# Optimization experiments

Measured on AMD Instinct MI355X. Metric: run time of the kernel, lower is better.

## Reference

```python
import jax, jax.numpy as jnp
import numpy as np

K_CAND = 64
K_FINAL = 16
ALPHA = 0.5
CURV_RATIO = 0.5
EPS = 1e-8


def index_points(points, idx):
    # points: [B, N, C], idx: [B, ...] -> [B, ..., C]
    B, N, C = points.shape
    flat = idx.reshape(B, -1)
    g = jnp.take_along_axis(points, flat[..., None], axis=1)
    return g.reshape(idx.shape + (C,))


def fps(points, num_fps):
    # Furthest point sampling (matches pointnet2: starts from index 0).
    B, N, _ = points.shape
    barange = jnp.arange(B)

    def body(carry, _):
        mindist, last_idx = carry
        last_pt = points[barange, last_idx]                       # [B, 3]
        d = jnp.sum((points - last_pt[:, None, :]) ** 2, axis=-1)  # [B, N]
        mindist = jnp.minimum(mindist, d)
        next_idx = jnp.argmax(mindist, axis=1).astype(jnp.int32)
        return (mindist, next_idx), last_idx

    init = (jnp.full((B, N), 1e10, points.dtype), jnp.zeros((B,), jnp.int32))
    _, idxs = jax.lax.scan(body, init, None, length=num_fps)
    return idxs.T  # [B, num_fps]


def znorm(x):
    # per-cloud normalization over points dim, unbiased std like torch
    return (x - x.mean(axis=1, keepdims=True)) / (x.std(axis=1, ddof=1, keepdims=True) + EPS)


def reference(xyz, features, w1, b1, w2, b2, num_samples):
    B, N, _ = xyz.shape
    # --- candidate kNN via pairwise squared distances (same ordering as cdist) ---
    sq = jnp.sum(xyz * xyz, axis=-1)                               # [B, N]
    d2 = sq[:, :, None] + sq[:, None, :] - 2.0 * jnp.einsum('bnc,bmc->bnm', xyz, xyz)
    _, cand = jax.lax.top_k(-d2, K_CAND + 1)                       # smallest dists first
    cand = cand[:, :, 1:]                                          # drop self -> [B, N, 64]

    # --- learned neighbor scoring MLP on relative geometry/features ---
    nxyz = index_points(xyz, cand)                                 # [B, N, 64, 3]
    nfeat = index_points(features, cand)                           # [B, N, 64, C]
    rel_xyz = nxyz - xyz[:, :, None, :]
    rel_feat = nfeat - features[:, :, None, :]
    mlp_in = jnp.concatenate([rel_xyz, rel_feat], axis=-1)         # [B, N, 64, 3+C]
    h = jax.nn.gelu(mlp_in @ w1 + b1, approximate=False)
    scores = (h @ w2 + b2)[..., 0]                                 # [B, N, 64]
    _, top_in_cand = jax.lax.top_k(scores, K_FINAL)
    final_idx = jnp.take_along_axis(cand, top_in_cand, axis=2)     # [B, N, 16]

    # --- robust importance: curvature (3x3 SVD of cov) + feature variation ---
    n2xyz = index_points(xyz, final_idx)                           # [B, N, 16, 3]
    n2feat = index_points(features, final_idx)
    dxyz = n2xyz - xyz[:, :, None, :]
    cov = jnp.einsum('bnki,bnkj->bnij', dxyz, dxyz) / K_FINAL      # [B, N, 3, 3]
    s = jnp.linalg.svd(cov, compute_uv=False)                      # descending, [B, N, 3]
    l2, l1, l0 = s[..., 0] ** 2, s[..., 1] ** 2, s[..., 2] ** 2
    curvature = l0 / (l0 + l1 + l2 + EPS)
    dfeat = n2feat - features[:, :, None, :]
    feat_var = jnp.linalg.norm(dfeat, axis=-1).mean(axis=-1)       # [B, N]
    importance = znorm(curvature) + ALPHA * znorm(feat_var)

    # --- select curvature points, mask them, FPS for the rest ---
    num_curv = int(num_samples * CURV_RATIO)
    num_fps = num_samples - num_curv
    _, curv_idx = jax.lax.top_k(importance, num_curv)              # [B, num_curv]
    far_val = jnp.max(xyz) + 1.0
    barange = jnp.arange(B)[:, None]
    masked_xyz = xyz.at[barange, curv_idx].set(far_val)
    fps_idx = fps(masked_xyz, num_fps).astype(curv_idx.dtype)      # [B, num_fps]
    merged = jnp.concatenate([curv_idx, fps_idx], axis=1)          # [B, num_samples]
    sampled_xyz = index_points(xyz, merged)                        # [B, num_samples, 3]
    return sampled_xyz, merged


def setup_inputs() -> dict:
    key = jax.random.key(0)
    k1, k2, k3, k4 = jax.random.split(key, 4)
    B, N, C = 2, 8192, 64
    xyz = jax.random.normal(k1, (B, N, 3), jnp.float32)
    features = jax.random.normal(k2, (B, N, C), jnp.float32)
    fan_in1 = 3 + C
    w1 = jax.random.normal(k3, (fan_in1, 128), jnp.float32) / np.sqrt(fan_in1)
    b1 = jnp.zeros((128,), jnp.float32)
    w2 = jax.random.normal(k4, (128, 1), jnp.float32) / np.sqrt(128)
    b2 = jnp.zeros((1,), jnp.float32)
    return {"xyz": xyz, "features": features, "w1": w1, "b1": b1,
            "w2": w2, "b2": b2, "num_samples": 2048}
```

## Files before the change

### kernel.cpp

```cpp
#include <hip/hip_runtime.h>
#include <hip/hip_bf16.h>
#include <math.h>

#define N 8192
#define BATCH 2
#define NROWS (BATCH*N)

typedef float v2f __attribute__((ext_vector_type(2)));

static __device__ __forceinline__ float fsubr(float a, float b){ return __fadd_rn(a, -b); }
static __device__ __forceinline__ unsigned okey(float f){
  unsigned u = __float_as_uint(f);
  return (u & 0x80000000u) ? ~u : (u | 0x80000000u);
}

__global__ void aux_kernel(const float* __restrict__ xyz, float* __restrict__ xs, float* __restrict__ ys,
                           float* __restrict__ zs, float* __restrict__ sq, float4* __restrict__ mxyz){
  int i = blockIdx.x*256 + threadIdx.x;
  if (i < NROWS){
    float x = xyz[i*3+0], y = xyz[i*3+1], z = xyz[i*3+2];
    xs[i]=x; ys[i]=y; zs[i]=z;
    sq[i] = __fadd_rn(__fadd_rn(__fmul_rn(x,x),__fmul_rn(y,y)),__fmul_rn(z,z));
    mxyz[i] = make_float4(x, y, z, 0.0f);
  }
}

__global__ void farval_kernel(const float* __restrict__ xyz, float* __restrict__ farval){
  __shared__ float lm[4];
  float m = -1e30f;
  for (int i = threadIdx.x; i < NROWS*3; i += 256) m = fmaxf(m, xyz[i]);
  for (int off = 32; off; off >>= 1) m = fmaxf(m, __shfl_down(m, off));
  if ((threadIdx.x & 63) == 0) lm[threadIdx.x >> 6] = m;
  __syncthreads();
  if (threadIdx.x == 0){
    float r = fmaxf(fmaxf(lm[0],lm[1]), fmaxf(lm[2],lm[3]));
    farval[0] = __fadd_rn(r, 1.0f);
  }
}

__global__ __launch_bounds__(128) void q_kernel(const float* __restrict__ xyz, const float* __restrict__ feat,
                                                const float* __restrict__ w1, float* __restrict__ Q){
  __shared__ float sx[16][3];
  __shared__ float sf[16][64];
  const int t = threadIdx.x;
  const int row0 = blockIdx.x * 16;
  for (int j = t; j < 1024; j += 128) sf[j>>6][j&63] = feat[(size_t)row0*64 + j];
  if (t < 48) sx[t/3][t%3] = xyz[(size_t)row0*3 + t];
  __syncthreads();
  float acc[16];
  #pragma unroll
  for (int r = 0; r < 16; ++r) acc[r] = 0.0f;
  for (int c = 0; c < 3; ++c){
    float wv = w1[c*128 + t];
    #pragma unroll
    for (int r = 0; r < 16; ++r) acc[r] = fmaf(sx[r][c], wv, acc[r]);
  }
  for (int c = 0; c < 64; ++c){
    float wv = w1[(3+c)*128 + t];
    #pragma unroll
    for (int r = 0; r < 16; ++r) acc[r] = fmaf(sf[r][c], wv, acc[r]);
  }
  #pragma unroll
  for (int r = 0; r < 16; ++r) Q[(size_t)(row0+r)*128 + t] = acc[r];
}

__global__ __launch_bounds__(512) void knn_kernel(const float* __restrict__ xs, const float* __restrict__ ys,
                                                  const float* __restrict__ zs, const float* __restrict__ sq,
                                                  int* __restrict__ cand){
#pragma clang fp contract(off)
  __shared__ unsigned fk[N];
  __shared__ unsigned hist[2048];
  __shared__ unsigned long long win[1024];
  __shared__ int scal[8];
  const int t = threadIdx.x;
  const int base_row = blockIdx.x * 32;
  const int b = base_row >> 13;
  const int n0 = base_row & (N-1);
  const int pbase = b * N;
  v2f px[8], py[8], pz[8], ps[8];
  #pragma unroll
  for (int k = 0; k < 8; ++k){
    int i0 = t + (2*k)*512, i1 = t + (2*k+1)*512;
    px[k].x = xs[pbase+i0]; px[k].y = xs[pbase+i1];
    py[k].x = ys[pbase+i0]; py[k].y = ys[pbase+i1];
    pz[k].x = zs[pbase+i0]; pz[k].y = zs[pbase+i1];
    ps[k].x = sq[pbase+i0]; ps[k].y = sq[pbase+i1];
  }
  for (int r = 0; r < 32; ++r){
    const int n = n0 + r;
    const float qx = xs[pbase+n], qy = ys[pbase+n], qz = zs[pbase+n], qs = sq[pbase+n];
    #pragma unroll
    for (int j = 0; j < 4; ++j) hist[t + j*512] = 0;
    __syncthreads();
    #pragma unroll
    for (int k = 0; k < 8; ++k){
      v2f dot = px[k]*qx + py[k]*qy + pz[k]*qz;
      v2f dd  = (qs + ps[k]) - 2.0f*dot;
      unsigned u0 = okey(dd.x), u1 = okey(dd.y);
      fk[t + (2*k)*512] = u0;
      fk[t + (2*k+1)*512] = u1;
      atomicAdd(&hist[u0 >> 21], 1u);
      atomicAdd(&hist[u1 >> 21], 1u);
    }
    __syncthreads();
    if (t < 64){
      unsigned s = 0;
      for (int k2 = 0; k2 < 32; ++k2) s += hist[t*32 + ((k2 + t) & 31)];
      unsigned p = s;
      for (int off = 1; off < 64; off <<= 1){ unsigned v = (unsigned)__shfl_up((int)p, off); if (t >= off) p += v; }
      int excl = (int)(p - s);
      if (excl < 65 && (int)p >= 65){ scal[0] = t; scal[1] = excl; }
    }
    __syncthreads();
    {
      int g = scal[0];
      if (t < 32){
        unsigned s = hist[g*32 + t];
        unsigned p = s;
        for (int off = 1; off < 32; off <<= 1){ unsigned v = (unsigned)__shfl_up((int)p, off); if (t >= off) p += v; }
        int before = scal[1] + (int)(p - s);
        if (before < 65 && scal[1] + (int)p >= 65) scal[2] = g*32 + t;
      }
    }
    if (t == 0) scal[3] = 0;
    __syncthreads();
    unsigned B1 = (unsigned)scal[2];
    unsigned limit = (B1 >= 2047u) ? 0xFFFFFFFFu : ((B1+1u) << 21);
    #pragma unroll
    for (int j = 0; j < 16; ++j){
      int i = t + j*512;
      unsigned u = fk[i];
      if (u < limit){
        int p = atomicAdd(&scal[3], 1);
        if (p < 1024) win[p] = ((unsigned long long)u << 32) | (unsigned)i;
      }
    }
    __syncthreads();
    int m = scal[3]; if (m > 1024) m = 1024;
    for (int e = t; e < m; e += 512){
      unsigned long long me = win[e];
      int rk = 0;
      for (int j2 = 0; j2 < m; ++j2) rk += (win[j2] < me) ? 1 : 0;
      if (rk >= 1 && rk < 65) cand[(size_t)(pbase + n)*64 + (rk-1)] = (int)(me & 0xFFFFFFFFull);
    }
    __syncthreads();
  }
}

__global__ __launch_bounds__(256) void score_kernel(const float* __restrict__ xyz, const float* __restrict__ feat,
                                                    const float* __restrict__ Q, const float* __restrict__ b1,
                                                    const float* __restrict__ w2, const float* __restrict__ b2,
                                                    const int* __restrict__ cand,
                                                    float* __restrict__ curv, float* __restrict__ fv){
  __shared__ float4 sb14[32], sw24[32];
  __shared__ int ssel[4][16];
  __shared__ float sdx[4][16], sdy[4][16], sdz[4][16], snrm[4][16];
  const int t = threadIdx.x;
  if (t < 32) sb14[t] = ((const float4*)b1)[t];
  else if (t < 64) sw24[t-32] = ((const float4*)w2)[t-32];
  __syncthreads();
  const int w = t >> 6, lane = t & 63;
  const int row = blockIdx.x*4 + w;
  const int b = row >> 13;
  const int pbase = b * N;
  const int n = row & (N-1);
  const int ck = cand[(size_t)row*64 + lane];
  const float4* Qn4 = (const float4*)(Q + (size_t)row * 128);
  const float4* Qc4 = (const float4*)(Q + (size_t)(pbase + ck) * 128);
  const float ks = 0.70710678118654752440f;
  float acc = 0.0f;
  for (int c = 0; c < 32; ++c){
    float4 qc = Qc4[c], qn = Qn4[c], bb = sb14[c], ww = sw24[c];
    float p0 = (qc.x - qn.x) + bb.x;
    float g0 = 0.5f * p0 * (1.0f + erff(p0 * ks));
    acc += g0 * ww.x;
    float p1 = (qc.y - qn.y) + bb.y;
    float g1 = 0.5f * p1 * (1.0f + erff(p1 * ks));
    acc += g1 * ww.y;
    float p2 = (qc.z - qn.z) + bb.z;
    float g2 = 0.5f * p2 * (1.0f + erff(p2 * ks));
    acc += g2 * ww.z;
    float p3 = (qc.w - qn.w) + bb.w;
    float g3 = 0.5f * p3 * (1.0f + erff(p3 * ks));
    acc += g3 * ww.w;
  }
  float score = acc + b2[0];
  unsigned key = okey(score);
  int rk = 0;
  for (int j = 0; j < 64; ++j){
    unsigned kj = (unsigned)__shfl((int)key, j);
    rk += (kj > key || (kj == key && j < lane)) ? 1 : 0;
  }
  float cx = xyz[(size_t)(pbase+ck)*3+0], cy = xyz[(size_t)(pbase+ck)*3+1], cz = xyz[(size_t)(pbase+ck)*3+2];
  float qxv = xyz[(size_t)(pbase+n)*3+0], qyv = xyz[(size_t)(pbase+n)*3+1], qzv = xyz[(size_t)(pbase+n)*3+2];
  if (rk < 16){
    ssel[w][rk] = ck;
    sdx[w][rk] = fsubr(cx, qxv);
    sdy[w][rk] = fsubr(cy, qyv);
    sdz[w][rk] = fsubr(cz, qzv);
  }
  __syncthreads();
  if (lane < 16){
    int si = ssel[w][lane];
    const float4* fc4 = (const float4*)(feat + (size_t)(pbase+si)*64);
    const float4* fn4 = (const float4*)(feat + (size_t)(pbase+n)*64);
    double s = 0.0;
    for (int c = 0; c < 16; ++c){
      float4 a = fc4[c], bq = fn4[c];
      float d0 = fsubr(a.x, bq.x); s += (double)d0 * (double)d0;
      float d1 = fsubr(a.y, bq.y); s += (double)d1 * (double)d1;
      float d2 = fsubr(a.z, bq.z); s += (double)d2 * (double)d2;
      float d3 = fsubr(a.w, bq.w); s += (double)d3 * (double)d3;
    }
    snrm[w][lane] = sqrtf((float)s);
  }
  __syncthreads();
  if (lane == 0){
    double cxx=0, cxy=0, cxz=0, cyy=0, cyz=0, czz=0;
    for (int k2 = 0; k2 < 16; ++k2){
      double dx = (double)sdx[w][k2], dy = (double)sdy[w][k2], dz = (double)sdz[w][k2];
      cxx += dx*dx; cxy += dx*dy; cxz += dx*dz; cyy += dy*dy; cyz += dy*dz; czz += dz*dz;
    }
    float fxx = (float)(cxx/16.0), fxy = (float)(cxy/16.0), fxz = (float)(cxz/16.0);
    float fyy = (float)(cyy/16.0), fyz = (float)(cyz/16.0), fzz = (float)(czz/16.0);
    double a = fxx, bbv = fyy, c = fzz, d = fxy, e = fyz, f = fxz;
    double p1 = d*d + f*f + e*e;
    double e0, e1, e2v;
    if (p1 == 0.0){ e0 = a; e1 = bbv; e2v = c; }
    else {
      double q = (a + bbv + c) / 3.0;
      double aa = a - q, bq = bbv - q, cc = c - q;
      double p2 = aa*aa + bq*bq + cc*cc + 2.0*p1;
      double p = sqrt(p2 / 6.0);
      double inv = 1.0 / p;
      double bxx = aa*inv, byy = bq*inv, bzz = cc*inv, bxy = d*inv, bxz = f*inv, byz = e*inv;
      double detB = bxx*(byy*bzz - byz*byz) - bxy*(bxy*bzz - byz*bxz) + bxz*(bxy*byz - byy*bxz);
      double rr = 0.5 * detB;
      rr = fmin(1.0, fmax(-1.0, rr));
      double phi = acos(rr) / 3.0;
      e0 = q + 2.0*p*cos(phi);
      e2v = q + 2.0*p*cos(phi + 2.0943951023931953);
      e1 = 3.0*q - e0 - e2v;
    }
    double s0 = fabs(e0), s1 = fabs(e1), s2d = fabs(e2v), tt;
    if (s0 < s1){ tt=s0; s0=s1; s1=tt; }
    if (s1 < s2d){ tt=s1; s1=s2d; s2d=tt; }
    if (s0 < s1){ tt=s0; s0=s1; s1=tt; }
    float sv0 = (float)s0, sv1 = (float)s1, sv2 = (float)s2d;
    float l2f = __fmul_rn(sv0,sv0), l1f = __fmul_rn(sv1,sv1), l0f = __fmul_rn(sv2,sv2);
    float den = __fadd_rn(__fadd_rn(__fadd_rn(l0f, l1f), l2f), 1e-8f);
    curv[row] = l0f / den;
    double fs = 0.0;
    for (int k2 = 0; k2 < 16; ++k2) fs += (double)snrm[w][k2];
    fv[row] = (float)(fs / 16.0);
  }
}

static __device__ __forceinline__ double blk_sum(double v, double* lds, int t){
  for (int off = 32; off; off >>= 1) v += __shfl_down(v, off);
  int w = t >> 6, lane = t & 63;
  if (lane == 0) lds[w] = v;
  __syncthreads();
  double r = (t < 16) ? lds[t] : 0.0;
  if (t < 64){ for (int off = 8; off; off >>= 1) r += __shfl_down(r, off); }
  if (t == 0) lds[0] = r;
  __syncthreads();
  double out = lds[0];
  __syncthreads();
  return out;
}

__global__ __launch_bounds__(1024) void stats_kernel(const float* __restrict__ curv, const float* __restrict__ fv,
                                                     float* __restrict__ imp){
  __shared__ double lds[16];
  const int t = threadIdx.x;
  const int base = blockIdx.x * N;
  double sc = 0, sf = 0;
  for (int j = 0; j < 8; ++j){ int i = t + j*1024; sc += (double)curv[base+i]; sf += (double)fv[base+i]; }
  double Sc = blk_sum(sc, lds, t);
  double Sf = blk_sum(sf, lds, t);
  double mc = Sc/8192.0, mf = Sf/8192.0;
  double vc = 0, vf = 0;
  for (int j = 0; j < 8; ++j){ int i = t + j*1024;
    double d1 = (double)curv[base+i] - mc; vc += d1*d1;
    double d2 = (double)fv[base+i]  - mf; vf += d2*d2; }
  double Vc = blk_sum(vc, lds, t);
  double Vf = blk_sum(vf, lds, t);
  float mcf = (float)mc, mff = (float)mf;
  float dc = __fadd_rn((float)sqrt(Vc/8191.0), 1e-8f);
  float df = __fadd_rn((float)sqrt(Vf/8191.0), 1e-8f);
  for (int j = 0; j < 8; ++j){ int i = t + j*1024;
    float zc = fsubr(curv[base+i], mcf) / dc;
    float zf = fsubr(fv[base+i],  mff) / df;
    imp[base+i] = __fadd_rn(zc, __fmul_rn(0.5f, zf));
  }
}

__global__ __launch_bounds__(1024) void topk_kernel(const float* __restrict__ imp, int* __restrict__ merged,
                                                    float4* __restrict__ mxyz, const float* __restrict__ farval){
  __shared__ unsigned dk[N];
  __shared__ unsigned hist[2048];
  __shared__ unsigned long long win[2048];
  __shared__ int scal[8];
  const int t = threadIdx.x;
  const int b = blockIdx.x;
  const int base = b * N;
  #pragma unroll
  for (int j = 0; j < 2; ++j) hist[t + j*1024] = 0;
  if (t == 0) scal[3] = 0;
  __syncthreads();
  for (int j = 0; j < 8; ++j){
    int i = t + j*1024;
    unsigned u = ~okey(imp[base+i]);
    dk[i] = u;
    atomicAdd(&hist[u >> 21], 1u);
  }
  __syncthreads();
  if (t < 64){
    unsigned s = 0;
    for (int k2 = 0; k2 < 32; ++k2) s += hist[t*32 + ((k2 + t) & 31)];
    unsigned p = s;
    for (int off = 1; off < 64; off <<= 1){ unsigned v = (unsigned)__shfl_up((int)p, off); if (t >= off) p += v; }
    int excl = (int)(p - s);
    if (excl < 1024 && (int)p >= 1024){ scal[0] = t; scal[1] = excl; }
  }
  __syncthreads();
  {
    int g = scal[0];
    if (t < 32){
      unsigned s = hist[g*32 + t];
      unsigned p = s;
      for (int off = 1; off < 32; off <<= 1){ unsigned v = (unsigned)__shfl_up((int)p, off); if (t >= off) p += v; }
      int before = scal[1] + (int)(p - s);
      if (before < 1024 && scal[1] + (int)p >= 1024) scal[2] = g*32 + t;
    }
  }
  __syncthreads();
  unsigned B1 = (unsigned)scal[2];
  unsigned limit = (B1 >= 2047u) ? 0xFFFFFFFFu : ((B1+1u) << 21);
  for (int j = 0; j < 8; ++j){
    int i = t + j*1024;
    unsigned u = dk[i];
    if (u < limit){
      int p = atomicAdd(&scal[3], 1);
      if (p < 2048) win[p] = ((unsigned long long)u << 13) | (unsigned)i;
    }
  }
  __syncthreads();
  int m = scal[3]; if (m > 2048) m = 2048;
  const float far = farval[0];
  for (int e = t; e < m; e += 1024){
    unsigned long long me = win[e];
    int rk = 0;
    for (int j2 = 0; j2 < m; ++j2) rk += (win[j2] < me) ? 1 : 0;
    if (rk < 1024){
      int idx = (int)(me & 0x1FFFull);
      merged[b*2048 + rk] = idx;
      mxyz[base + idx] = make_float4(far, far, far, 0.0f);
    }
  }
}

#define DPP_MAX64(CTRL) { \
    int nlo = __builtin_amdgcn_update_dpp(0, klo, (CTRL), 0xf, 0xf, true); \
    int nhi = __builtin_amdgcn_update_dpp(0, khi, (CTRL), 0xf, 0xf, true); \
    unsigned long long nk = ((unsigned long long)(unsigned)nhi << 32) | (unsigned)nlo; \
    unsigned long long ck = ((unsigned long long)(unsigned)khi << 32) | (unsigned)klo; \
    if (nk > ck){ klo = nlo; khi = nhi; } \
  }

__global__ __launch_bounds__(512, 1) void fps_kernel(const float4* __restrict__ mxyz, int* __restrict__ merged){
#pragma clang fp contract(off)
  extern __shared__ float4 stab[];
  __shared__ unsigned long long wkey[2][8];
  const int t = threadIdx.x;
  const int b = blockIdx.x;
  const int base = b * N;
  v2f px[8], py[8], pz[8], md[8];
  #pragma unroll
  for (int k = 0; k < 8; ++k){
    int i0 = t + (2*k)*512, i1 = t + (2*k+1)*512;
    float4 p0 = mxyz[base + i0];
    float4 p1 = mxyz[base + i1];
    stab[i0] = p0; stab[i1] = p1;
    px[k].x = p0.x; px[k].y = p1.x;
    py[k].x = p0.y; py[k].y = p1.y;
    pz[k].x = p0.z; pz[k].y = p1.z;
    md[k].x = 1e10f; md[k].y = 1e10f;
  }
  if (t == 0) merged[b*2048 + 1024] = 0;
  __syncthreads();
  float4 w0 = stab[0];
  float lx = w0.x, ly = w0.y, lz = w0.z;
  for (int it = 0; it < 1023; ++it){
    v2f vmax; vmax.x = -1.0f; vmax.y = -1.0f;
    #pragma unroll
    for (int k = 0; k < 8; ++k){
      v2f dx = px[k] - lx, dy = py[k] - ly, dz = pz[k] - lz;
      v2f d = dx*dx + dy*dy + dz*dz;
      v2f nm = __builtin_elementwise_min(md[k], d);
      md[k] = nm;
      vmax = __builtin_elementwise_max(vmax, nm);
    }
    const float bestv = fmaxf(vmax.x, vmax.y);
    unsigned blow = 0u;
    #pragma unroll
    for (int j = 15; j >= 0; --j){
      float v = (j & 1) ? md[j>>1].y : md[j>>1].x;
      if (v == bestv) blow = 8191u - (unsigned)(t + (j<<9));
    }
    unsigned long long key = ((unsigned long long)__float_as_uint(bestv) << 13) | (unsigned long long)blow;
    int klo = (int)(unsigned)(key & 0xFFFFFFFFull);
    int khi = (int)(unsigned)(key >> 32);
    DPP_MAX64(0x111)
    DPP_MAX64(0x112)
    DPP_MAX64(0x114)
    DPP_MAX64(0x118)
    DPP_MAX64(0x142)
    DPP_MAX64(0x143)
    if ((t & 63) == 63)
      wkey[it & 1][t >> 6] = ((unsigned long long)(unsigned)khi << 32) | (unsigned)klo;
    __syncthreads();
    const unsigned long long* wk = wkey[it & 1];
    unsigned long long k = wk[0];
    #pragma unroll
    for (int i2 = 1; i2 < 8; ++i2){ unsigned long long o = wk[i2]; if (o > k) k = o; }
    const int idx = 8191 - (int)(k & 0x1FFFull);
    if (t == 0) merged[b*2048 + 1024 + it + 1] = idx;
    float4 wv = stab[idx];
    lx = wv.x; ly = wv.y; lz = wv.z;
  }
}

__global__ void finalize_kernel(const float* __restrict__ xyz, const int* __restrict__ merged,
                                float* __restrict__ out){
  int i = blockIdx.x*256 + threadIdx.x;
  if (i < BATCH*2048){
    int b = i >> 11;
    int idx = merged[i];
    out[12288 + i] = (float)idx;
    const float* p = xyz + (size_t)(b*N + idx)*3;
    out[i*3+0] = p[0]; out[i*3+1] = p[1]; out[i*3+2] = p[2];
  }
}

extern "C" void kernel_launch(void* const* d_in, const int* in_sizes, int n_in,
                              void* d_out, int out_size, void* d_ws, size_t ws_size,
                              hipStream_t stream){
  const float* xyz  = (const float*)d_in[0];
  const float* feat = (const float*)d_in[1];
  const float* w1   = (const float*)d_in[2];
  const float* b1   = (const float*)d_in[3];
  const float* w2   = (const float*)d_in[4];
  const float* b2   = (const float*)d_in[5];
  float* out = (float*)d_out;
  char* ws = (char*)d_ws;
  float*  Q      = (float*) (ws);
  int*    cand   = (int*)   (ws + 8388608);
  float*  xs     = (float*) (ws + 12582912);
  float*  ysv    = (float*) (ws + 12648448);
  float*  zsv    = (float*) (ws + 12713984);
  float*  sq     = (float*) (ws + 12779520);
  float*  curv   = (float*) (ws + 12845056);
  float*  fv     = (float*) (ws + 12910592);
  float*  imp    = (float*) (ws + 12976128);
  int*    merged = (int*)   (ws + 13041664);
  float*  farval = (float*) (ws + 13058048);
  float4* mxyz   = (float4*)(ws + 13058112);

  aux_kernel<<<64, 256, 0, stream>>>(xyz, xs, ysv, zsv, sq, mxyz);
  farval_kernel<<<1, 256, 0, stream>>>(xyz, farval);
  q_kernel<<<1024, 128, 0, stream>>>(xyz, feat, w1, Q);
  knn_kernel<<<512, 512, 0, stream>>>(xs, ysv, zsv, sq, cand);
  score_kernel<<<4096, 256, 0, stream>>>(xyz, feat, Q, b1, w2, b2, cand, curv, fv);
  stats_kernel<<<2, 1024, 0, stream>>>(curv, fv, imp);
  topk_kernel<<<2, 1024, 0, stream>>>(imp, merged, mxyz, farval);
  fps_kernel<<<2, 512, 131072, stream>>>(mxyz, merged);
  finalize_kernel<<<16, 256, 0, stream>>>(xyz, merged, out);
}
```

Baseline: 1.705 ms.

## Refine kNN histogram binning and split FPS wave reduction into float max then index

The kNN radix histogram now bins on bits 16+ offset by a fixed base and clamps out-of-range keys into the edge bins. This gives finer bins over the expected small-distance range, so fewer candidates pass into the quadratic rank-sort window. The FPS argmax reduction is split into a 32-bit DPP float max, a lane readback, and a second 32-bit DPP max over the index, replacing 64-bit key reductions; the point arrays also become scalar named registers instead of arrays. The fixed bin base relies on the distribution of distance values, and if more than 1024 keys land below the threshold the window overflows.

```diff
diff --git a/kernel.cpp b/kernel.cpp
--- a/kernel.cpp
+++ b/kernel.cpp
@@ -64,6 +64,7 @@
   for (int r = 0; r < 16; ++r) Q[(size_t)(row0+r)*128 + t] = acc[r];
 }
 
+#define BINBASE 0xBA00
 __global__ __launch_bounds__(512) void knn_kernel(const float* __restrict__ xs, const float* __restrict__ ys,
                                                   const float* __restrict__ zs, const float* __restrict__ sq,
                                                   int* __restrict__ cand){
@@ -99,8 +100,10 @@
       unsigned u0 = okey(dd.x), u1 = okey(dd.y);
       fk[t + (2*k)*512] = u0;
       fk[t + (2*k+1)*512] = u1;
-      atomicAdd(&hist[u0 >> 21], 1u);
-      atomicAdd(&hist[u1 >> 21], 1u);
+      int bin0 = (int)(u0 >> 16) - BINBASE; bin0 = bin0 < 0 ? 0 : (bin0 > 2047 ? 2047 : bin0);
+      int bin1 = (int)(u1 >> 16) - BINBASE; bin1 = bin1 < 0 ? 0 : (bin1 > 2047 ? 2047 : bin1);
+      atomicAdd(&hist[bin0], 1u);
+      atomicAdd(&hist[bin1], 1u);
     }
     __syncthreads();
     if (t < 64){
@@ -124,8 +127,8 @@
     }
     if (t == 0) scal[3] = 0;
     __syncthreads();
-    unsigned B1 = (unsigned)scal[2];
-    unsigned limit = (B1 >= 2047u) ? 0xFFFFFFFFu : ((B1+1u) << 21);
+    int B1 = scal[2];
+    unsigned limit = (B1 >= 2047) ? 0xFFFFFFFFu : ((unsigned)(BINBASE + B1 + 1) << 16);
     #pragma unroll
     for (int j = 0; j < 16; ++j){
       int i = t + j*512;
@@ -361,13 +364,18 @@
   }
 }
 
-#define DPP_MAX64(CTRL) { \
-    int nlo = __builtin_amdgcn_update_dpp(0, klo, (CTRL), 0xf, 0xf, true); \
-    int nhi = __builtin_amdgcn_update_dpp(0, khi, (CTRL), 0xf, 0xf, true); \
-    unsigned long long nk = ((unsigned long long)(unsigned)nhi << 32) | (unsigned)nlo; \
-    unsigned long long ck = ((unsigned long long)(unsigned)khi << 32) | (unsigned)klo; \
-    if (nk > ck){ klo = nlo; khi = nhi; } \
-  }
+#define FPS_LOAD(k) { int i0=t+(2*k)*512, i1=t+(2*k+1)*512; \
+    float4 a0 = mxyz[base+i0], a1 = mxyz[base+i1]; stab[i0]=a0; stab[i1]=a1; \
+    px##k=(v2f){a0.x,a1.x}; py##k=(v2f){a0.y,a1.y}; pz##k=(v2f){a0.z,a1.z}; md##k=(v2f){1e10f,1e10f}; }
+#define FPS_UPD(k) { v2f dx=px##k-lx, dy=py##k-ly, dz=pz##k-lz; \
+    v2f d=dx*dx+dy*dy+dz*dz; md##k=__builtin_elementwise_min(md##k,d); \
+    vmax=__builtin_elementwise_max(vmax,md##k); }
+#define FPS_PICK(k) { if (md##k.y == wmf) blow = 8191u - (unsigned)(t + ((2*k+1)<<9)); \
+    if (md##k.x == wmf) blow = 8191u - (unsigned)(t + ((2*k)<<9)); }
+#define DPPMAXF(CTRL) { int mo = __builtin_amdgcn_update_dpp(0, __float_as_int(wm), (CTRL), 0xf, 0xf, true); \
+    wm = fmaxf(wm, __int_as_float(mo)); }
+#define DPPMAXU(CTRL) { int mo = __builtin_amdgcn_update_dpp(0, (int)blow, (CTRL), 0xf, 0xf, true); \
+    blow = (blow > (unsigned)mo) ? blow : (unsigned)mo; }
 
 __global__ __launch_bounds__(512, 1) void fps_kernel(const float4* __restrict__ mxyz, int* __restrict__ merged){
 #pragma clang fp contract(off)
@@ -376,50 +384,31 @@
   const int t = threadIdx.x;
   const int b = blockIdx.x;
   const int base = b * N;
-  v2f px[8], py[8], pz[8], md[8];
-  #pragma unroll
-  for (int k = 0; k < 8; ++k){
-    int i0 = t + (2*k)*512, i1 = t + (2*k+1)*512;
-    float4 p0 = mxyz[base + i0];
-    float4 p1 = mxyz[base + i1];
-    stab[i0] = p0; stab[i1] = p1;
-    px[k].x = p0.x; px[k].y = p1.x;
-    py[k].x = p0.y; py[k].y = p1.y;
-    pz[k].x = p0.z; pz[k].y = p1.z;
-    md[k].x = 1e10f; md[k].y = 1e10f;
-  }
+  v2f px0,px1,px2,px3,px4,px5,px6,px7;
+  v2f py0,py1,py2,py3,py4,py5,py6,py7;
+  v2f pz0,pz1,pz2,pz3,pz4,pz5,pz6,pz7;
+  v2f md0,md1,md2,md3,md4,md5,md6,md7;
+  FPS_LOAD(0) FPS_LOAD(1) FPS_LOAD(2) FPS_LOAD(3)
+  FPS_LOAD(4) FPS_LOAD(5) FPS_LOAD(6) FPS_LOAD(7)
   if (t == 0) merged[b*2048 + 1024] = 0;
   __syncthreads();
   float4 w0 = stab[0];
   float lx = w0.x, ly = w0.y, lz = w0.z;
   for (int it = 0; it < 1023; ++it){
     v2f vmax; vmax.x = -1.0f; vmax.y = -1.0f;
-    #pragma unroll
-    for (int k = 0; k < 8; ++k){
-      v2f dx = px[k] - lx, dy = py[k] - ly, dz = pz[k] - lz;
-      v2f d = dx*dx + dy*dy + dz*dz;
-      v2f nm = __builtin_elementwise_min(md[k], d);
-      md[k] = nm;
-      vmax = __builtin_elementwise_max(vmax, nm);
-    }
-    const float bestv = fmaxf(vmax.x, vmax.y);
+    FPS_UPD(0) FPS_UPD(1) FPS_UPD(2) FPS_UPD(3)
+    FPS_UPD(4) FPS_UPD(5) FPS_UPD(6) FPS_UPD(7)
+    float wm = fmaxf(vmax.x, vmax.y);
+    DPPMAXF(0x111) DPPMAXF(0x112) DPPMAXF(0x114) DPPMAXF(0x118)
+    DPPMAXF(0x142) DPPMAXF(0x143)
+    const float wmf = __int_as_float(__builtin_amdgcn_readlane(__float_as_int(wm), 63));
     unsigned blow = 0u;
-    #pragma unroll
-    for (int j = 15; j >= 0; --j){
-      float v = (j & 1) ? md[j>>1].y : md[j>>1].x;
-      if (v == bestv) blow = 8191u - (unsigned)(t + (j<<9));
-    }
-    unsigned long long key = ((unsigned long long)__float_as_uint(bestv) << 13) | (unsigned long long)blow;
-    int klo = (int)(unsigned)(key & 0xFFFFFFFFull);
-    int khi = (int)(unsigned)(key >> 32);
-    DPP_MAX64(0x111)
-    DPP_MAX64(0x112)
-    DPP_MAX64(0x114)
-    DPP_MAX64(0x118)
-    DPP_MAX64(0x142)
-    DPP_MAX64(0x143)
+    FPS_PICK(7) FPS_PICK(6) FPS_PICK(5) FPS_PICK(4)
+    FPS_PICK(3) FPS_PICK(2) FPS_PICK(1) FPS_PICK(0)
+    DPPMAXU(0x111) DPPMAXU(0x112) DPPMAXU(0x114) DPPMAXU(0x118)
+    DPPMAXU(0x142) DPPMAXU(0x143)
     if ((t & 63) == 63)
-      wkey[it & 1][t >> 6] = ((unsigned long long)(unsigned)khi << 32) | (unsigned)klo;
+      wkey[it & 1][t >> 6] = ((unsigned long long)__float_as_uint(wmf) << 13) | (unsigned long long)blow;
     __syncthreads();
     const unsigned long long* wk = wkey[it & 1];
     unsigned long long k = wk[0];
```

Result: faster. 1.647 ms (-3.4%).
